# Optimization experiments

Measured on AMD Instinct MI355X. Metric: run time of the kernel, lower is better.

## Reference

```python
import jax, jax.numpy as jnp
import numpy as np

D = 128; H = 4; DK = D // H; ZN = 64; V = 8

def _silu(x):
    return x * jax.nn.sigmoid(x)

def _mlp3(x, w1, b1, w2, b2, w3, b3):
    h = _silu(x @ w1 + b1)
    h = _silu(h @ w2 + b2)
    return h @ w3 + b3

def _snorm(x):
    # StaticLayerNorm: center, divide by unbiased std (torch .std default ddof=1)
    c = x - jnp.mean(x, axis=-1, keepdims=True)
    std = jnp.sqrt(jnp.sum(c * c, axis=-1, keepdims=True) / (x.shape[-1] - 1))
    std = jnp.where(std == 0, 1.0, std)
    return c / std

def setup_inputs():
    key = jax.random.key(0)
    ks = list(jax.random.split(key, 40)); ki = iter(ks)
    xs = (6.0 / (DK + D)) ** 0.5
    inp = {}
    inp["latent"] = jax.random.normal(next(ki), (ZN, D, V, V, V), jnp.float32)
    inp["nodes"] = jax.random.normal(next(ki), (ZN, D), jnp.float32)
    inp["t"] = jax.random.uniform(next(ki), (ZN,), jnp.float32)
    for nm in ("qw", "kw", "vw"):
        inp[nm] = jax.random.uniform(next(ki), (H, D, DK), jnp.float32, -xs, xs)
    for nm in ("qb", "kb", "vb"):
        inp[nm] = jnp.zeros((H, DK), jnp.float32)
    inp["ow"] = jax.random.normal(next(ki), (D, D), jnp.float32) * (1.0 / D) ** 0.5
    for pre, dout in (("an_gb", 2 * D), ("an_a", D), ("fn_gb", 2 * D), ("fn_a", D)):
        inp[pre + "_w1"] = jax.random.normal(next(ki), (D, D), jnp.float32) * 0.05
        inp[pre + "_b1"] = jnp.zeros((D,), jnp.float32)
        inp[pre + "_w2"] = jax.random.normal(next(ki), (D, D), jnp.float32) * 0.05
        inp[pre + "_b2"] = jnp.zeros((D,), jnp.float32)
        inp[pre + "_w3"] = jax.random.normal(next(ki), (D, dout), jnp.float32) * 0.05
        inp[pre + "_b3"] = jnp.zeros((dout,), jnp.float32)
    return inp

def reference(latent, nodes, t, qw, kw, vw, qb, kb, vb, ow,
              an_gb_w1, an_gb_b1, an_gb_w2, an_gb_b2, an_gb_w3, an_gb_b3,
              an_a_w1, an_a_b1, an_a_w2, an_a_b2, an_a_w3, an_a_b3,
              fn_gb_w1, fn_gb_b1, fn_gb_w2, fn_gb_b2, fn_gb_w3, fn_gb_b3,
              fn_a_w1, fn_a_b1, fn_a_w2, fn_a_b2, fn_a_w3, fn_a_b3):
    b, d, vx, vy, vz = latent.shape
    n = vx * vy * vz
    x = latent.reshape(b, d, n).transpose(0, 2, 1)  # [b, n, d]
    cond = nodes[:, None, :] + t[:, None, None]     # [b, 1, d]
    gb1 = _mlp3(cond, an_gb_w1, an_gb_b1, an_gb_w2, an_gb_b2, an_gb_w3, an_gb_b3)
    g1, be1 = jnp.split(gb1, 2, axis=-1)
    al1 = _mlp3(cond, an_a_w1, an_a_b1, an_a_w2, an_a_b2, an_a_w3, an_a_b3)
    gb2 = _mlp3(cond, fn_gb_w1, fn_gb_b1, fn_gb_w2, fn_gb_b2, fn_gb_w3, fn_gb_b3)
    g2, be2 = jnp.split(gb2, 2, axis=-1)
    al2 = _mlp3(cond, fn_a_w1, fn_a_b1, fn_a_w2, fn_a_b2, fn_a_w3, fn_a_b3)
    # FAITHFUL BUG REPRO: source unpacks adaLN's (gamma, beta, alpha) as (alpha, gamma, beta)
    alpha1, gamma1, beta1 = g1, be1, al1
    alpha2, gamma2, beta2 = g2, be2, al2
    x2 = gamma1 * _snorm(x) + beta1
    dk = d // qw.shape[0]
    Q = jnp.einsum('bnd,hdk->bhnk', x2, qw) + qb[None, :, None, :]
    K = jnp.einsum('bnd,hdk->bhnk', x2, kw) + kb[None, :, None, :]
    Vv = jnp.einsum('bnd,hdk->bhnk', x2, vw) + vb[None, :, None, :]
    S = jnp.einsum('bhnk,bhmk->bhnm', Q, K) / (dk ** 0.5)
    P = jax.nn.softmax(S, axis=-1)
    O = jnp.einsum('bhnm,bhmk->bhnk', P, Vv)
    O = O.transpose(0, 2, 3, 1).reshape(b, n, d)  # matches torch permute(0,2,3,1).reshape
    attn = O @ ow
    x = x + alpha1 * attn
    x2 = gamma2 * _snorm(x) + beta2
    x = x + alpha2 * x2  # NOTE: source forward never applies self.ffn (dead module)
    return x.transpose(0, 2, 1).reshape(b, d, vx, vy, vz)
```

## Files before the change

kernel.cpp:

```cpp
#include <hip/hip_runtime.h>
#include <hip/hip_bf16.h>
#include <math.h>


#define NB 64

typedef __attribute__((ext_vector_type(8))) short bf16x8;
typedef __attribute__((ext_vector_type(4))) float f32x4;

__device__ __forceinline__ float silu_f(float x) { return x / (1.0f + __expf(-x)); }
__device__ __forceinline__ unsigned short f2bf(float x) {
    __hip_bfloat16 h = __float2bfloat16(x);
    return *reinterpret_cast<unsigned short*>(&h);
}

__global__ void __launch_bounds__(128) k_cond(
    const float* __restrict__ nodes, const float* __restrict__ tv,
    const float* __restrict__ w10, const float* __restrict__ b10,
    const float* __restrict__ w20, const float* __restrict__ b20,
    const float* __restrict__ w30, const float* __restrict__ b30,
    const float* __restrict__ w11, const float* __restrict__ b11,
    const float* __restrict__ w21, const float* __restrict__ b21,
    const float* __restrict__ w31, const float* __restrict__ b31,
    const float* __restrict__ w12, const float* __restrict__ b12,
    const float* __restrict__ w22, const float* __restrict__ b22,
    const float* __restrict__ w32, const float* __restrict__ b32,
    const float* __restrict__ w13, const float* __restrict__ b13,
    const float* __restrict__ w23, const float* __restrict__ b23,
    const float* __restrict__ w33, const float* __restrict__ b33,
    float* __restrict__ mods)
{
    int blk = blockIdx.x;
    int b = blk >> 2, m = blk & 3;
    const float* W1 = m==0?w10 : m==1?w11 : m==2?w12 : w13;
    const float* B1 = m==0?b10 : m==1?b11 : m==2?b12 : b13;
    const float* W2 = m==0?w20 : m==1?w21 : m==2?w22 : w23;
    const float* B2 = m==0?b20 : m==1?b21 : m==2?b22 : b23;
    const float* W3 = m==0?w30 : m==1?w31 : m==2?w32 : w33;
    const float* B3 = m==0?b30 : m==1?b31 : m==2?b32 : b33;
    int dout256 = (m == 0 || m == 2);
    int slot = (m==0)?0 : (m==1)?2 : (m==2)?3 : 5;

    __shared__ float xs[128], h1[128], h2[128];
    int t = threadIdx.x;
    xs[t] = nodes[b*128 + t] + tv[b];
    __syncthreads();

    float acc = B1[t];
    for (int i = 0; i < 128; i++) acc += xs[i] * W1[i*128 + t];
    h1[t] = silu_f(acc);
    __syncthreads();

    acc = B2[t];
    for (int i = 0; i < 128; i++) acc += h1[i] * W2[i*128 + t];
    h2[t] = silu_f(acc);
    __syncthreads();

    if (dout256) {
        float a0 = B3[t], a1 = B3[t + 128];
        for (int i = 0; i < 128; i++) {
            float h = h2[i];
            a0 += h * W3[i*256 + t];
            a1 += h * W3[i*256 + t + 128];
        }
        mods[((size_t)b*6 + slot    )*128 + t] = a0;
        mods[((size_t)b*6 + slot + 1)*128 + t] = a1;
    } else {
        float a0 = B3[t];
        for (int i = 0; i < 128; i++) a0 += h2[i] * W3[i*128 + t];
        mods[((size_t)b*6 + slot)*128 + t] = a0;
    }
}

__global__ void __launch_bounds__(256, 1) k_norm_qkv(
    const float* __restrict__ latent, const float* __restrict__ mods,
    const float* __restrict__ qw, const float* __restrict__ kw, const float* __restrict__ vw,
    const float* __restrict__ qb, const float* __restrict__ kb, const float* __restrict__ vb,
    unsigned short* __restrict__ Qb, unsigned short* __restrict__ Kb,
    unsigned short* __restrict__ Vtb)
{
    __shared__ float xs[64*129];
    __shared__ unsigned short xb[64*136];
    __shared__ unsigned short WtS[128*136];
    __shared__ float g1s[128], be1s[128], mean_s[64], rstd_s[64];

    int blk = blockIdx.x;
    int b = blk >> 3, n0 = (blk & 7) * 64;
    int t = threadIdx.x;

    if (t < 128) {
        g1s[t]  = mods[((size_t)b*6 + 1)*128 + t];
        be1s[t] = mods[((size_t)b*6 + 2)*128 + t];
    }
    const float* lp = latent + (size_t)b*65536 + n0;
    for (int idx = t; idx < 8192; idx += 256) {
        int d = idx >> 6, j = idx & 63;
        xs[j*129 + d] = lp[(size_t)d*512 + j];
    }
    __syncthreads();

    {
        int row = t >> 2, sub = t & 3;
        float s = 0.f, ss = 0.f;
        const float* xr = &xs[row*129 + sub*32];
        #pragma unroll
        for (int i = 0; i < 32; i++) { float v = xr[i]; s += v; ss += v*v; }
        s += __shfl_xor(s, 1); ss += __shfl_xor(ss, 1);
        s += __shfl_xor(s, 2); ss += __shfl_xor(ss, 2);
        float mean = s * (1.0f/128.0f);
        float var = (ss - 128.0f*mean*mean) * (1.0f/127.0f);
        var = var < 0.f ? 0.f : var;
        float sd = sqrtf(var);
        mean_s[row] = mean;
        rstd_s[row] = (sd == 0.f) ? 1.f : 1.f/sd;
    }
    __syncthreads();

    for (int idx = t; idx < 8192; idx += 256) {
        int j = idx >> 7, d = idx & 127;
        float v = xs[j*129 + d];
        xb[j*136 + d] = f2bf(g1s[d]*((v - mean_s[j]) * rstd_s[j]) + be1s[d]);
    }
    __syncthreads();

    int w = t >> 6, lane = t & 63, lo = lane & 15, hi = lane >> 4;

    bf16x8 af[4];
    #pragma unroll
    for (int kc = 0; kc < 4; kc++)
        af[kc] = *(const bf16x8*)(xb + (w*16 + lo)*136 + kc*32 + hi*8);

    const f32x4 zero = {0.f, 0.f, 0.f, 0.f};
    const float qscale = 0.17677669529663687f * 1.4426950408889634f;

    #pragma unroll 1
    for (int ph = 0; ph < 3; ph++) {
        const float* wp = ph==0 ? qw : (ph==1 ? kw : vw);
        __syncthreads();
        for (int idx = t; idx < 16384; idx += 256) {
            int kk = idx & 31, d = (idx >> 5) & 127, h = idx >> 12;
            WtS[(h*32 + kk)*136 + d] = f2bf(wp[idx]);
        }
        __syncthreads();

        for (int nt = 0; nt < 8; nt++) {
            f32x4 acc = zero;
            #pragma unroll
            for (int kc = 0; kc < 4; kc++) {
                bf16x8 bf = *(const bf16x8*)(WtS + (nt*16 + lo)*136 + kc*32 + hi*8);
                acc = __builtin_amdgcn_mfma_f32_16x16x32_bf16(af[kc], bf, acc, 0, 0, 0);
            }
            int c = nt*16 + lo, h = c >> 5, kk = c & 31;
            size_t bh = (size_t)(b*4 + h);
            if (ph == 0) {
                float bias = qb[c];
                #pragma unroll
                for (int j = 0; j < 4; j++) {
                    int n = n0 + w*16 + hi*4 + j;
                    Qb[(bh*512 + n)*32 + kk] = f2bf((acc[j] + bias) * qscale);
                }
            } else if (ph == 1) {
                float bias = kb[c];
                #pragma unroll
                for (int j = 0; j < 4; j++) {
                    int n = n0 + w*16 + hi*4 + j;
                    Kb[(bh*512 + n)*32 + kk] = f2bf(acc[j] + bias);
                }
            } else {
                float bias = vb[c];
                #pragma unroll
                for (int j = 0; j < 4; j++) {
                    int nl = w*16 + hi*4 + j;
                    xb[c*68 + nl] = f2bf(acc[j] + bias);
                }
            }
        }
    }
    __syncthreads();
    for (int idx = t; idx < 8192; idx += 256) {
        int c = idx >> 6, j = idx & 63;
        int h = c >> 5, kk = c & 31;
        size_t bh = (size_t)(b*4 + h);
        Vtb[(bh*32 + kk)*512 + n0 + j] = xb[c*68 + j];
    }
}

__global__ void __launch_bounds__(512, 4) k_attn(
    const unsigned short* __restrict__ Qb, const unsigned short* __restrict__ Kb,
    const unsigned short* __restrict__ Vtb, unsigned short* __restrict__ Ob)
{
    __shared__ unsigned short KsS[512*32];
    __shared__ unsigned short VsS[32*512];

    int blk = blockIdx.x;
    int bh = blk >> 1, qhalf = blk & 1;
    int t = threadIdx.x;

    const unsigned short* kgp = Kb + (size_t)bh*512*32;
    const unsigned short* vgp = Vtb + (size_t)bh*32*512;
    for (int idx = t; idx < 2048; idx += 512)
        *(bf16x8*)(KsS + idx*8) = *(const bf16x8*)(kgp + idx*8);
    for (int idx = t; idx < 2048; idx += 512) {
        int r = idx >> 6, cch = idx & 63;
        *(bf16x8*)(VsS + r*512 + ((cch*8) ^ ((r&7)<<3))) =
            *(const bf16x8*)(vgp + r*512 + cch*8);
    }
    __syncthreads();

    int w = t >> 6, lane = t & 63, lo = lane & 15, hi = lane >> 4;
    const unsigned short* qbase = Qb + (size_t)bh*512*32;
    const f32x4 zero = {0.f, 0.f, 0.f, 0.f};
    int b = bh >> 2, h = bh & 3;

    const unsigned short* Vl0 = VsS + lo*512;
    const unsigned short* Vl1 = VsS + (16 + lo)*512;
    int swz = (lo & 7) << 3;
    int srcA = lo + 32*(hi & 1);

    for (int qt = 0; qt < 2; ++qt) {
        int q0 = qhalf*256 + w*32 + qt*16;
        bf16x8 qa = *(const bf16x8*)(qbase + (size_t)(q0 + lo)*32 + hi*8);

        float m = -1e30f, sum = 0.f;
        f32x4 oa = zero, ob = zero;

        #pragma unroll 1
        for (int ch = 0; ch < 4; ++ch) {
            f32x4 s8[8];
            #pragma unroll
            for (int kt = 0; kt < 8; ++kt) {
                bf16x8 kf = *(const bf16x8*)(KsS + ((ch*8 + kt)*16 + lo)*32 + hi*8);
                s8[kt] = __builtin_amdgcn_mfma_f32_16x16x32_bf16(kf, qa, zero, 0, 0, 0);
            }

            float cm = -1e30f;
            #pragma unroll
            for (int kt = 0; kt < 8; ++kt)
                cm = fmaxf(cm, fmaxf(fmaxf(s8[kt][0], s8[kt][1]), fmaxf(s8[kt][2], s8[kt][3])));
            cm = fmaxf(cm, __shfl_xor(cm, 16));
            cm = fmaxf(cm, __shfl_xor(cm, 32));
            float nm = fmaxf(m, cm);
            float sc = __builtin_amdgcn_exp2f(m - nm);
            sum *= sc;
            #pragma unroll
            for (int j = 0; j < 4; ++j) { oa[j] *= sc; ob[j] *= sc; }
            m = nm;

            unsigned pw0c[8], pw1c[8];
            #pragma unroll
            for (int kt = 0; kt < 8; ++kt) {
                float p0 = __builtin_amdgcn_exp2f(s8[kt][0] - nm);
                float p1 = __builtin_amdgcn_exp2f(s8[kt][1] - nm);
                float p2 = __builtin_amdgcn_exp2f(s8[kt][2] - nm);
                float p3 = __builtin_amdgcn_exp2f(s8[kt][3] - nm);
                sum += (p0 + p1) + (p2 + p3);
                pw0c[kt] = (unsigned)f2bf(p0) | ((unsigned)f2bf(p1) << 16);
                pw1c[kt] = (unsigned)f2bf(p2) | ((unsigned)f2bf(p3) << 16);
            }

            #pragma unroll
            for (int kt2 = 0; kt2 < 4; ++kt2) {
                unsigned e0 = pw0c[2*kt2],     e1 = pw1c[2*kt2];
                unsigned o0 = pw0c[2*kt2 + 1], o1 = pw1c[2*kt2 + 1];
                unsigned ae0 = (unsigned)__shfl((int)e0, srcA, 64);
                unsigned ae1 = (unsigned)__shfl((int)e1, srcA, 64);
                unsigned ao0 = (unsigned)__shfl((int)o0, srcA, 64);
                unsigned ao1 = (unsigned)__shfl((int)o1, srcA, 64);
                unsigned be0 = (unsigned)__shfl((int)e0, srcA + 16, 64);
                unsigned be1 = (unsigned)__shfl((int)e1, srcA + 16, 64);
                unsigned bo0 = (unsigned)__shfl((int)o0, srcA + 16, 64);
                unsigned bo1 = (unsigned)__shfl((int)o1, srcA + 16, 64);
                union { unsigned u[4]; bf16x8 v; } pb;
                pb.u[0] = (hi < 2) ? ae0 : ao0;
                pb.u[1] = (hi < 2) ? ae1 : ao1;
                pb.u[2] = (hi < 2) ? be0 : bo0;
                pb.u[3] = (hi < 2) ? be1 : bo1;
                int off = (((ch*4 + kt2)*32) + hi*8) ^ swz;
                bf16x8 v0 = *(const bf16x8*)(Vl0 + off);
                bf16x8 v1 = *(const bf16x8*)(Vl1 + off);
                oa = __builtin_amdgcn_mfma_f32_16x16x32_bf16(v0, pb.v, oa, 0, 0, 0);
                ob = __builtin_amdgcn_mfma_f32_16x16x32_bf16(v1, pb.v, ob, 0, 0, 0);
            }
        }

        sum += __shfl_xor(sum, 16);
        sum += __shfl_xor(sum, 32);

        float inv = 1.f / sum;
        unsigned short* op = Ob + ((size_t)(b*512 + q0 + lo))*128 + h;
        #pragma unroll
        for (int j = 0; j < 4; ++j) {
            op[(hi*4 + j)*4]       = f2bf(oa[j] * inv);
            op[(16 + hi*4 + j)*4]  = f2bf(ob[j] * inv);
        }
    }
}

__global__ void __launch_bounds__(256, 2) k_out(
    const float* __restrict__ latent, const unsigned short* __restrict__ Ob,
    const float* __restrict__ ow, const float* __restrict__ mods,
    float* __restrict__ outp)
{
    __shared__ unsigned short owT[128*136];
    __shared__ float xs[64*129];
    __shared__ float a1s[128], a2s[128], g2s[128], b2s[128];
    __shared__ float mean_s[64], rstd_s[64];

    int blk = blockIdx.x;
    int b = blk >> 3, n0 = (blk & 7) * 64;
    int t = threadIdx.x;

    if (t < 128) {
        a1s[t] = mods[((size_t)b*6 + 0)*128 + t];
        a2s[t] = mods[((size_t)b*6 + 3)*128 + t];
        g2s[t] = mods[((size_t)b*6 + 4)*128 + t];
        b2s[t] = mods[((size_t)b*6 + 5)*128 + t];
    }
    for (int idx = t; idx < 16384; idx += 256) {
        int i = idx >> 7, c = idx & 127;
        owT[c*136 + i] = f2bf(ow[idx]);
    }
    const float* lp = latent + (size_t)b*65536 + n0;
    for (int idx = t; idx < 8192; idx += 256) {
        int d = idx >> 6, j = idx & 63;
        xs[j*129 + d] = lp[(size_t)d*512 + j];
    }
    __syncthreads();

    int w = t >> 6, lane = t & 63, lo = lane & 15, hi = lane >> 4;

    const unsigned short* arow = Ob + ((size_t)(b*512 + n0 + w*16 + lo))*128;
    bf16x8 af[4];
    #pragma unroll
    for (int kc = 0; kc < 4; kc++)
        af[kc] = *(const bf16x8*)(arow + kc*32 + hi*8);

    const f32x4 zero = {0.f, 0.f, 0.f, 0.f};
    for (int nt = 0; nt < 8; nt++) {
        f32x4 acc = zero;
        #pragma unroll
        for (int kc = 0; kc < 4; kc++) {
            bf16x8 bf = *(const bf16x8*)(owT + (nt*16 + lo)*136 + kc*32 + hi*8);
            acc = __builtin_amdgcn_mfma_f32_16x16x32_bf16(af[kc], bf, acc, 0, 0, 0);
        }
        int c = nt*16 + lo;
        #pragma unroll
        for (int j = 0; j < 4; j++) {
            int nl = w*16 + hi*4 + j;
            xs[nl*129 + c] += a1s[c] * acc[j];
        }
    }
    __syncthreads();

    {
        int row = t >> 2, sub = t & 3;
        float s = 0.f, ss = 0.f;
        const float* xr = &xs[row*129 + sub*32];
        #pragma unroll
        for (int i = 0; i < 32; i++) { float v = xr[i]; s += v; ss += v*v; }
        s += __shfl_xor(s, 1); ss += __shfl_xor(ss, 1);
        s += __shfl_xor(s, 2); ss += __shfl_xor(ss, 2);
        float mean = s * (1.0f/128.0f);
        float var = (ss - 128.0f*mean*mean) * (1.0f/127.0f);
        var = var < 0.f ? 0.f : var;
        float sd = sqrtf(var);
        mean_s[row] = mean;
        rstd_s[row] = (sd == 0.f) ? 1.f : 1.f/sd;
    }
    __syncthreads();

    float* outb = outp + (size_t)b*65536 + n0;
    for (int idx = t; idx < 8192; idx += 256) {
        int d = idx >> 6, j = idx & 63;
        float v = xs[j*129 + d];
        float nv = (v - mean_s[j]) * rstd_s[j];
        outb[(size_t)d*512 + j] = v + a2s[d]*(g2s[d]*nv + b2s[d]);
    }
}

extern "C" void kernel_launch(void* const* d_in, const int* in_sizes, int n_in,
                              void* d_out, int out_size, void* d_ws, size_t ws_size,
                              hipStream_t stream) {
    const float* latent = (const float*)d_in[0];
    const float* nodes  = (const float*)d_in[1];
    const float* tv     = (const float*)d_in[2];
    const float* qw     = (const float*)d_in[3];
    const float* kw     = (const float*)d_in[4];
    const float* vw     = (const float*)d_in[5];
    const float* qb     = (const float*)d_in[6];
    const float* kb     = (const float*)d_in[7];
    const float* vb     = (const float*)d_in[8];
    const float* owp    = (const float*)d_in[9];

    const float* mw[24];
    for (int i = 0; i < 24; i++) mw[i] = (const float*)d_in[10 + i];

    char* wsb = (char*)d_ws;
    unsigned short* Qb  = (unsigned short*)(wsb);
    unsigned short* Kb  = (unsigned short*)(wsb + 8388608);
    unsigned short* Vtb = (unsigned short*)(wsb + 16777216);
    unsigned short* Ob  = (unsigned short*)(wsb + 25165824);
    float* mods = (float*)(wsb + 33554432);

    float* outp = (float*)d_out;

    k_cond<<<dim3(NB*4), dim3(128), 0, stream>>>(
        nodes, tv,
        mw[0], mw[1], mw[2], mw[3], mw[4], mw[5],
        mw[6], mw[7], mw[8], mw[9], mw[10], mw[11],
        mw[12], mw[13], mw[14], mw[15], mw[16], mw[17],
        mw[18], mw[19], mw[20], mw[21], mw[22], mw[23],
        mods);

    k_norm_qkv<<<dim3(NB*8), dim3(256), 0, stream>>>(
        latent, mods, qw, kw, vw, qb, kb, vb, Qb, Kb, Vtb);

    k_attn<<<dim3(NB*4*2), dim3(512), 0, stream>>>(Qb, Kb, Vtb, Ob);

    k_out<<<dim3(NB*8), dim3(256), 0, stream>>>(latent, Ob, owp, mods, outp);
}
```

Before: 225.0 us.

## Pre-convert weights to bf16 once and read from global in QKV/out kernels

Adds a small prep kernel that converts and transposes the Q/K/V and output projection weights to bf16 once per call, instead of every block re-converting them into shared memory. k_norm_qkv now loads latent straight into registers for the norm, packs bf16 pairs, and drops the large fp32 staging buffer. Shared memory use falls, so launch bounds are raised to allow more blocks per CU. The cost is an extra kernel launch, and B-operand fragments now come from global/L2 rather than LDS.

```diff
diff --git a/kernel.cpp b/kernel.cpp
--- a/kernel.cpp
+++ b/kernel.cpp
@@ -12,6 +12,23 @@
 __device__ __forceinline__ unsigned short f2bf(float x) {
     __hip_bfloat16 h = __float2bfloat16(x);
     return *reinterpret_cast<unsigned short*>(&h);
+}
+
+__global__ void __launch_bounds__(256) k_prep(
+    const float* __restrict__ qw, const float* __restrict__ kw,
+    const float* __restrict__ vw, const float* __restrict__ ow,
+    unsigned short* __restrict__ cT, unsigned short* __restrict__ owT)
+{
+    int idx = blockIdx.x*256 + threadIdx.x;
+    if (idx < 49152) {
+        int ph = idx >> 14, r = idx & 16383, c = r >> 7, d = r & 127;
+        int h = c >> 5, kk = c & 31;
+        const float* wp = ph==0 ? qw : (ph==1 ? kw : vw);
+        cT[idx] = f2bf(wp[h*4096 + d*32 + kk]);
+    } else {
+        int r = idx - 49152, c = r >> 7, i = r & 127;
+        owT[r] = f2bf(ow[i*128 + c]);
+    }
 }
 
 __global__ void __launch_bounds__(128) k_cond(
@@ -72,82 +89,66 @@
     }
 }
 
-__global__ void __launch_bounds__(256, 1) k_norm_qkv(
+__global__ void __launch_bounds__(256, 4) k_norm_qkv(
     const float* __restrict__ latent, const float* __restrict__ mods,
-    const float* __restrict__ qw, const float* __restrict__ kw, const float* __restrict__ vw,
+    const unsigned short* __restrict__ cT,
     const float* __restrict__ qb, const float* __restrict__ kb, const float* __restrict__ vb,
     unsigned short* __restrict__ Qb, unsigned short* __restrict__ Kb,
     unsigned short* __restrict__ Vtb)
 {
-    __shared__ float xs[64*129];
     __shared__ unsigned short xb[64*136];
-    __shared__ unsigned short WtS[128*136];
-    __shared__ float g1s[128], be1s[128], mean_s[64], rstd_s[64];
 
     int blk = blockIdx.x;
     int b = blk >> 3, n0 = (blk & 7) * 64;
     int t = threadIdx.x;
-
-    if (t < 128) {
-        g1s[t]  = mods[((size_t)b*6 + 1)*128 + t];
-        be1s[t] = mods[((size_t)b*6 + 2)*128 + t];
-    }
-    const float* lp = latent + (size_t)b*65536 + n0;
-    for (int idx = t; idx < 8192; idx += 256) {
-        int d = idx >> 6, j = idx & 63;
-        xs[j*129 + d] = lp[(size_t)d*512 + j];
-    }
-    __syncthreads();
-
-    {
-        int row = t >> 2, sub = t & 3;
-        float s = 0.f, ss = 0.f;
-        const float* xr = &xs[row*129 + sub*32];
-        #pragma unroll
-        for (int i = 0; i < 32; i++) { float v = xr[i]; s += v; ss += v*v; }
-        s += __shfl_xor(s, 1); ss += __shfl_xor(ss, 1);
-        s += __shfl_xor(s, 2); ss += __shfl_xor(ss, 2);
-        float mean = s * (1.0f/128.0f);
-        float var = (ss - 128.0f*mean*mean) * (1.0f/127.0f);
-        var = var < 0.f ? 0.f : var;
-        float sd = sqrtf(var);
-        mean_s[row] = mean;
-        rstd_s[row] = (sd == 0.f) ? 1.f : 1.f/sd;
-    }
-    __syncthreads();
-
-    for (int idx = t; idx < 8192; idx += 256) {
-        int j = idx >> 7, d = idx & 127;
-        float v = xs[j*129 + d];
-        xb[j*136 + d] = f2bf(g1s[d]*((v - mean_s[j]) * rstd_s[j]) + be1s[d]);
+    int j = t >> 2, sub = t & 3;
+
+    const float* lp = latent + (size_t)b*65536 + n0 + j;
+    float lat[32];
+    #pragma unroll
+    for (int i = 0; i < 32; i++)
+        lat[i] = lp[(size_t)(sub*32 + i)*512];
+
+    float s = 0.f, ss = 0.f;
+    #pragma unroll
+    for (int i = 0; i < 32; i++) { s += lat[i]; ss += lat[i]*lat[i]; }
+    s += __shfl_xor(s, 1); ss += __shfl_xor(ss, 1);
+    s += __shfl_xor(s, 2); ss += __shfl_xor(ss, 2);
+    float mean = s * (1.0f/128.0f);
+    float var = (ss - 128.0f*mean*mean) * (1.0f/127.0f);
+    var = var < 0.f ? 0.f : var;
+    float sd = sqrtf(var);
+    float rstd = (sd == 0.f) ? 1.f : 1.f/sd;
+
+    const float* g1p  = mods + ((size_t)b*6 + 1)*128 + sub*32;
+    const float* be1p = mods + ((size_t)b*6 + 2)*128 + sub*32;
+    unsigned int* xbw = (unsigned int*)xb + j*68 + sub*16;
+    #pragma unroll
+    for (int i2 = 0; i2 < 16; i2++) {
+        float v0 = g1p[2*i2]   * ((lat[2*i2]   - mean)*rstd) + be1p[2*i2];
+        float v1 = g1p[2*i2+1] * ((lat[2*i2+1] - mean)*rstd) + be1p[2*i2+1];
+        xbw[i2] = (unsigned)f2bf(v0) | ((unsigned)f2bf(v1) << 16);
     }
     __syncthreads();
 
     int w = t >> 6, lane = t & 63, lo = lane & 15, hi = lane >> 4;
-
     bf16x8 af[4];
     #pragma unroll
     for (int kc = 0; kc < 4; kc++)
         af[kc] = *(const bf16x8*)(xb + (w*16 + lo)*136 + kc*32 + hi*8);
+    __syncthreads();
 
     const f32x4 zero = {0.f, 0.f, 0.f, 0.f};
     const float qscale = 0.17677669529663687f * 1.4426950408889634f;
 
     #pragma unroll 1
     for (int ph = 0; ph < 3; ph++) {
-        const float* wp = ph==0 ? qw : (ph==1 ? kw : vw);
-        __syncthreads();
-        for (int idx = t; idx < 16384; idx += 256) {
-            int kk = idx & 31, d = (idx >> 5) & 127, h = idx >> 12;
-            WtS[(h*32 + kk)*136 + d] = f2bf(wp[idx]);
-        }
-        __syncthreads();
-
+        const unsigned short* ct = cT + ph*16384;
         for (int nt = 0; nt < 8; nt++) {
             f32x4 acc = zero;
             #pragma unroll
             for (int kc = 0; kc < 4; kc++) {
-                bf16x8 bf = *(const bf16x8*)(WtS + (nt*16 + lo)*136 + kc*32 + hi*8);
+                bf16x8 bf = *(const bf16x8*)(ct + (nt*16 + lo)*128 + kc*32 + hi*8);
                 acc = __builtin_amdgcn_mfma_f32_16x16x32_bf16(af[kc], bf, acc, 0, 0, 0);
             }
             int c = nt*16 + lo, h = c >> 5, kk = c & 31;
@@ -155,33 +156,33 @@
             if (ph == 0) {
                 float bias = qb[c];
                 #pragma unroll
-                for (int j = 0; j < 4; j++) {
-                    int n = n0 + w*16 + hi*4 + j;
-                    Qb[(bh*512 + n)*32 + kk] = f2bf((acc[j] + bias) * qscale);
+                for (int jj = 0; jj < 4; jj++) {
+                    int n = n0 + w*16 + hi*4 + jj;
+                    Qb[(bh*512 + n)*32 + kk] = f2bf((acc[jj] + bias) * qscale);
                 }
             } else if (ph == 1) {
                 float bias = kb[c];
                 #pragma unroll
-                for (int j = 0; j < 4; j++) {
-                    int n = n0 + w*16 + hi*4 + j;
-                    Kb[(bh*512 + n)*32 + kk] = f2bf(acc[j] + bias);
+                for (int jj = 0; jj < 4; jj++) {
+                    int n = n0 + w*16 + hi*4 + jj;
+                    Kb[(bh*512 + n)*32 + kk] = f2bf(acc[jj] + bias);
                 }
             } else {
                 float bias = vb[c];
                 #pragma unroll
-                for (int j = 0; j < 4; j++) {
-                    int nl = w*16 + hi*4 + j;
-                    xb[c*68 + nl] = f2bf(acc[j] + bias);
+                for (int jj = 0; jj < 4; jj++) {
+                    int nl = w*16 + hi*4 + jj;
+                    xb[c*68 + nl] = f2bf(acc[jj] + bias);
                 }
             }
         }
     }
     __syncthreads();
     for (int idx = t; idx < 8192; idx += 256) {
-        int c = idx >> 6, j = idx & 63;
+        int c = idx >> 6, jj = idx & 63;
         int h = c >> 5, kk = c & 31;
         size_t bh = (size_t)(b*4 + h);
-        Vtb[(bh*32 + kk)*512 + n0 + j] = xb[c*68 + j];
+        Vtb[(bh*32 + kk)*512 + n0 + jj] = xb[c*68 + jj];
     }
 }
 
@@ -243,7 +244,7 @@
             float sc = __builtin_amdgcn_exp2f(m - nm);
             sum *= sc;
             #pragma unroll
-            for (int j = 0; j < 4; ++j) { oa[j] *= sc; ob[j] *= sc; }
+            for (int jj = 0; jj < 4; ++jj) { oa[jj] *= sc; ob[jj] *= sc; }
             m = nm;
 
             unsigned pw0c[8], pw1c[8];
@@ -289,19 +290,18 @@
         float inv = 1.f / sum;
         unsigned short* op = Ob + ((size_t)(b*512 + q0 + lo))*128 + h;
         #pragma unroll
-        for (int j = 0; j < 4; ++j) {
-            op[(hi*4 + j)*4]       = f2bf(oa[j] * inv);
-            op[(16 + hi*4 + j)*4]  = f2bf(ob[j] * inv);
-        }
-    }
-}
-
-__global__ void __launch_bounds__(256, 2) k_out(
+        for (int jj = 0; jj < 4; ++jj) {
+            op[(hi*4 + jj)*4]       = f2bf(oa[jj] * inv);
+            op[(16 + hi*4 + jj)*4]  = f2bf(ob[jj] * inv);
+        }
+    }
+}
+
+__global__ void __launch_bounds__(256, 4) k_out(
     const float* __restrict__ latent, const unsigned short* __restrict__ Ob,
-    const float* __restrict__ ow, const float* __restrict__ mods,
+    const unsigned short* __restrict__ owT, const float* __restrict__ mods,
     float* __restrict__ outp)
 {
-    __shared__ unsigned short owT[128*136];
     __shared__ float xs[64*129];
     __shared__ float a1s[128], a2s[128], g2s[128], b2s[128];
     __shared__ float mean_s[64], rstd_s[64];
@@ -316,14 +316,10 @@
         g2s[t] = mods[((size_t)b*6 + 4)*128 + t];
         b2s[t] = mods[((size_t)b*6 + 5)*128 + t];
     }
-    for (int idx = t; idx < 16384; idx += 256) {
-        int i = idx >> 7, c = idx & 127;
-        owT[c*136 + i] = f2bf(ow[idx]);
-    }
     const float* lp = latent + (size_t)b*65536 + n0;
     for (int idx = t; idx < 8192; idx += 256) {
-        int d = idx >> 6, j = idx & 63;
-        xs[j*129 + d] = lp[(size_t)d*512 + j];
+        int d = idx >> 6, jj = idx & 63;
+        xs[jj*129 + d] = lp[(size_t)d*512 + jj];
     }
     __syncthreads();
 
@@ -340,14 +336,14 @@
         f32x4 acc = zero;
         #pragma unroll
         for (int kc = 0; kc < 4; kc++) {
-            bf16x8 bf = *(const bf16x8*)(owT + (nt*16 + lo)*136 + kc*32 + hi*8);
+            bf16x8 bf = *(const bf16x8*)(owT + (nt*16 + lo)*128 + kc*32 + hi*8);
             acc = __builtin_amdgcn_mfma_f32_16x16x32_bf16(af[kc], bf, acc, 0, 0, 0);
         }
         int c = nt*16 + lo;
         #pragma unroll
-        for (int j = 0; j < 4; j++) {
-            int nl = w*16 + hi*4 + j;
-            xs[nl*129 + c] += a1s[c] * acc[j];
+        for (int jj = 0; jj < 4; jj++) {
+            int nl = w*16 + hi*4 + jj;
+            xs[nl*129 + c] += a1s[c] * acc[jj];
         }
     }
     __syncthreads();
@@ -371,10 +367,10 @@
 
     float* outb = outp + (size_t)b*65536 + n0;
     for (int idx = t; idx < 8192; idx += 256) {
-        int d = idx >> 6, j = idx & 63;
-        float v = xs[j*129 + d];
-        float nv = (v - mean_s[j]) * rstd_s[j];
-        outb[(size_t)d*512 + j] = v + a2s[d]*(g2s[d]*nv + b2s[d]);
+        int d = idx >> 6, jj = idx & 63;
+        float v = xs[jj*129 + d];
+        float nv = (v - mean_s[jj]) * rstd_s[jj];
+        outb[(size_t)d*512 + jj] = v + a2s[d]*(g2s[d]*nv + b2s[d]);
     }
 }
 
@@ -400,9 +396,13 @@
     unsigned short* Kb  = (unsigned short*)(wsb + 8388608);
     unsigned short* Vtb = (unsigned short*)(wsb + 16777216);
     unsigned short* Ob  = (unsigned short*)(wsb + 25165824);
-    float* mods = (float*)(wsb + 33554432);
+    float* mods         = (float*)(wsb + 33554432);
+    unsigned short* cT  = (unsigned short*)(wsb + 33751040);
+    unsigned short* owT = (unsigned short*)(wsb + 33849344);
 
     float* outp = (float*)d_out;
+
+    k_prep<<<dim3(256), dim3(256), 0, stream>>>(qw, kw, vw, owp, cT, owT);
 
     k_cond<<<dim3(NB*4), dim3(128), 0, stream>>>(
         nodes, tv,
@@ -413,9 +413,9 @@
         mods);
 
     k_norm_qkv<<<dim3(NB*8), dim3(256), 0, stream>>>(
-        latent, mods, qw, kw, vw, qb, kb, vb, Qb, Kb, Vtb);
+        latent, mods, cT, qb, kb, vb, Qb, Kb, Vtb);
 
     k_attn<<<dim3(NB*4*2), dim3(512), 0, stream>>>(Qb, Kb, Vtb, Ob);
 
-    k_out<<<dim3(NB*8), dim3(256), 0, stream>>>(latent, Ob, owp, mods, outp);
-}
+    k_out<<<dim3(NB*8), dim3(256), 0, stream>>>(latent, Ob, owT, mods, outp);
+}
```

New measurement: 226.2 us. Within noise of the previous version (+0.6%).
